# Kernel optimization log

Hardware: AMD Instinct MI355X
Metric: run time of the kernel (lower is better)

The kernel has to match this reference:

```python
import jax, jax.numpy as jnp
import numpy as np

_D4_CODESZ = 4
_N_VECS = 1048576  # 2^20 4-dim vectors (~ one large LLM weight matrix shard)


def _code3_signs(i3, x):
    x = list(x)
    if i3 & (1 << 5):
        x[2] *= -1
    if i3 & (1 << 6):
        x[1] *= -1
    if sum(x) % 2 != 0:
        x[3] *= -1
    if i3 & (1 << 7):
        x = [-v for v in x]
    assert sum(x) % 2 == 0
    return x


def _code8_to_d4(i8):
    assert 0 <= i8 < 256
    i3 = i8 & (7 << 5)
    i8 = i8 & 31
    if i8 < 16:
        if i8 < 8:
            if i8 < 2:
                if i8 < 1:
                    return _code3_signs(i3, [0.5] * _D4_CODESZ)
                else:
                    return _code3_signs(i3, [1.5] * _D4_CODESZ)
            else:
                ibx = i8 >> 1
                if i8 & 1:
                    x = [0.5] * _D4_CODESZ
                    x[0] = 1.5
                    x[ibx] = 1.5
                else:
                    x = [1.5] * _D4_CODESZ
                    x[0] = 0.5
                    x[ibx] = 0.5
                return _code3_signs(i3, x)
        else:
            ibx = i8 & 3
            if i8 < 8 + 4:
                x = [0.5] * _D4_CODESZ
                x[ibx] = 1.5
            else:
                x = [1.5] * _D4_CODESZ
                x[ibx] = 0.5
            return _code3_signs(i3, x)
    elif i8 < 16 + 4:
        ibx = i8 & 3
        x = [0.5] * _D4_CODESZ
        x[ibx] = 2.5
        return _code3_signs(i3, x)
    else:
        ibx = i8 - 20
        ib4 = ibx & 3
        ib3 = ibx >> 2
        x = [0.5] * _D4_CODESZ
        x[ib4] = 1.5
        if ib3 >= ib4:
            ib3 += 1
        x[ib3] = 2.5
        return _code3_signs(i3, x)


def _build_d4_grid():
    cb = np.zeros((256, _D4_CODESZ), dtype=np.float32)
    for i in range(256):
        cb[i] = _code8_to_d4(i)
    return cb


def setup_inputs() -> dict:
    key = jax.random.key(0)
    X = jax.random.normal(key, (_N_VECS, _D4_CODESZ), dtype=jnp.float32)
    grid = jnp.asarray(_build_d4_grid())            # [256, 4] D4 lattice codebook
    grid_norm = jnp.sum(grid * grid, axis=1)        # [256] squared norms
    return {"X": X, "grid": grid, "grid_norm": grid_norm}


def reference(X, grid, grid_norm):
    # nearest-codeword by argmax of 2<x,g> - |g|^2 (equiv. to min ||x-g||^2)
    scores = 2.0 * jnp.einsum("nd,kd->nk", X, grid) - grid_norm  # [N, 256]
    Xqidx = jnp.argmax(scores, axis=1)                           # [N]
    return grid[Xqidx], Xqidx.astype(jnp.uint8)
```

## Files before the change

### kernel.cpp

```cpp
#include <hip/hip_runtime.h>
#include <math.h>

#define THREADS 256

#define MCP_LIST \
  0x00, 0x55, 0x50, 0x05, 0x44, 0x11, 0x14, 0x41, \
  0x01, 0x04, 0x10, 0x40, 0x54, 0x51, 0x45, 0x15, \
  0x02, 0x08, 0x20, 0x80, 0x09, 0x06, 0x12, 0x42, \
  0x21, 0x24, 0x18, 0x48, 0x81, 0x84, 0x90, 0x60

__device__ const unsigned d_MCP[32] = { MCP_LIST };
constexpr unsigned h_MCP[32] = { MCP_LIST };

__global__ __launch_bounds__(THREADS)
void d4_fast_kernel(const float* __restrict__ X, float* __restrict__ out,
                    unsigned char* __restrict__ flags, int n)
{
    const int i = blockIdx.x * blockDim.x + threadIdx.x;
    if (i >= n) return;

    const float4 xv = reinterpret_cast<const float4*>(X)[i];
    const float fx0 = xv.x, fx1 = xv.y, fx2 = xv.z, fx3 = xv.w;

    const double a0 = fabs((double)fx0), a1 = fabs((double)fx1);
    const double a2 = fabs((double)fx2), a3 = fabs((double)fx3);
    const double u0 = a0 + a0, u1 = a1 + a1, u2 = a2 + a2, u3 = a3 + a3;
    const double v0 = u0 + u0, v1 = u1 + u1, v2 = u2 + u2, v3 = u3 + u3;
    const double h0 = 0.5 * a0, h1 = 0.5 * a1, h2 = 0.5 * a2, h3 = 0.5 * a3;
    const double t0 = h0 + a0, t1 = h1 + a1, t2 = h2 + a2, t3 = h3 + a3;
    const double w0 = t0 + a0, w1 = t1 + a1, w2 = t2 + a2, w3 = t3 + a3;
    const double A = (a0 + a1) + (a2 + a3);

    const int s0 = (fx0 < 0.f) ? 1 : 0, s1 = (fx1 < 0.f) ? 1 : 0;
    const int s2 = (fx2 < 0.f) ? 1 : 0, s3 = (fx3 < 0.f) ? 1 : 0;
    const int qp = (s0 + s1 + s2 + s3) & 1;

    double best = -1e300, second = -1e300;
    int bi = 0;
#pragma unroll
    for (int p = 0; p < 32; ++p) {
        const unsigned mc = h_MCP[p];
        const int c0 = mc & 3, c1 = (mc >> 2) & 3, c2 = (mc >> 4) & 3, c3 = (mc >> 6) & 3;
        const int nsq = 1 + c0 * (c0 + 1) + c1 * (c1 + 1) + c2 * (c2 + 1) + c3 * (c3 + 1);

        double s = A - (double)nsq;
        if (c0 == 1) s += u0; else if (c0 == 2) s += v0;
        if (c1 == 1) s += u1; else if (c1 == 2) s += v1;
        if (c2 == 1) s += u2; else if (c2 == 2) s += v2;
        if (c3 == 1) s += u3; else if (c3 == 2) s += v3;

        const double q0 = (c0 == 0) ? h0 : ((c0 == 1) ? t0 : w0);
        const double q1 = (c1 == 0) ? h1 : ((c1 == 1) ? t1 : w1);
        const double q2 = (c2 == 0) ? h2 : ((c2 == 1) ? t2 : w2);
        const double q3 = (c3 == 0) ? h3 : ((c3 == 1) ? t3 : w3);
        const double minp = fmin(fmin(q0, q1), fmin(q2, q3));

        const int rp = (c0 + c1 + c2 + c3) & 1;
        const double eff = (rp != qp) ? (s - 4.0 * minp) : s;

        if (eff > best) { second = best; best = eff; bi = p; }
        else if (eff > second) { second = eff; }
    }

    const unsigned mc = d_MCP[bi];
    const int c0 = mc & 3, c1 = (mc >> 2) & 3, c2 = (mc >> 4) & 3, c3 = (mc >> 6) & 3;
    const int rp = (c0 + c1 + c2 + c3) & 1;
    const bool flip = (rp != qp);

    const double p0 = (c0 == 0) ? h0 : ((c0 == 1) ? t0 : w0);
    const double p1 = (c1 == 0) ? h1 : ((c1 == 1) ? t1 : w1);
    const double p2 = (c2 == 0) ? h2 : ((c2 == 1) ? t2 : w2);
    const double p3 = (c3 == 0) ? h3 : ((c3 == 1) ? t3 : w3);
    int f = 0; double mp = p0;
    if (p1 < mp) { mp = p1; f = 1; }
    if (p2 < mp) { mp = p2; f = 2; }
    if (p3 < mp) { mp = p3; f = 3; }

    const double m01 = fmin(p0, p1), M01 = fmax(p0, p1);
    const double m23 = fmin(p2, p3), M23 = fmax(p2, p3);
    const double q1v = fmin(m01, m23);
    const double q2v = fmin(fmax(m01, m23), fmin(M01, M23));

    const double within = flip ? 4.0 * (q2v - q1v) : 4.0 * (q1v + q2v);
    const double gap = fmin(best - second, within);
    const double delta = 4e-6 * (A + 1.0);
    flags[i] = (gap < delta) ? 1 : 0;

    const bool n0 = ((s0 != 0) != (flip && f == 0));
    const bool n1 = ((s1 != 0) != (flip && f == 1));
    const bool n2 = ((s2 != 0) != (flip && f == 2));
    const bool n3 = ((s3 != 0) != (flip && f == 3));

    const float m0 = 0.5f + (float)c0, m1 = 0.5f + (float)c1;
    const float m2 = 0.5f + (float)c2, m3 = 0.5f + (float)c3;
    float4 g;
    g.x = n0 ? -m0 : m0;
    g.y = n1 ? -m1 : m1;
    g.z = n2 ? -m2 : m2;
    g.w = n3 ? -m3 : m3;

    const int b7 = n0 ? 1 : 0;
    const int b6 = (n1 ? 1 : 0) ^ b7;
    const int b5 = (n2 ? 1 : 0) ^ b7;
    const int idx = bi | (b5 << 5) | (b6 << 6) | (b7 << 7);

    reinterpret_cast<float4*>(out)[i] = g;
    out[(size_t)4 * (size_t)n + (size_t)i] = (float)idx;
}

__global__ __launch_bounds__(THREADS)
void d4_exact_kernel(const float* __restrict__ X,
                     const float* __restrict__ grid,
                     const float* __restrict__ gnorm,
                     float* __restrict__ out,
                     const unsigned char* __restrict__ flags, int n)
{
    const int i = blockIdx.x * blockDim.x + threadIdx.x;
    if (i >= n) return;
    if (!flags[i]) return;

    const float4 xv = reinterpret_cast<const float4*>(X)[i];
    float best = -INFINITY;
    int bk = 0;
    for (int k = 0; k < 256; ++k) {
        const float g0 = grid[4 * k + 0], g1 = grid[4 * k + 1];
        const float g2 = grid[4 * k + 2], g3 = grid[4 * k + 3];
        float d = __fmul_rn(xv.x, g0);
        d = __fadd_rn(d, __fmul_rn(xv.y, g1));
        d = __fadd_rn(d, __fmul_rn(xv.z, g2));
        d = __fadd_rn(d, __fmul_rn(xv.w, g3));
        const float s = __fsub_rn(__fmul_rn(2.0f, d), gnorm[k]);
        if (s > best) { best = s; bk = k; }
    }
    float4 g;
    g.x = grid[4 * bk + 0]; g.y = grid[4 * bk + 1];
    g.z = grid[4 * bk + 2]; g.w = grid[4 * bk + 3];
    reinterpret_cast<float4*>(out)[i] = g;
    out[(size_t)4 * (size_t)n + (size_t)i] = (float)bk;
}

extern "C" void kernel_launch(void* const* d_in, const int* in_sizes, int n_in,
                              void* d_out, int out_size, void* d_ws, size_t ws_size,
                              hipStream_t stream)
{
    const float* X = (const float*)d_in[0];
    const float* grid = (const float*)d_in[1];
    const float* gnorm = (const float*)d_in[2];
    float* out = (float*)d_out;
    unsigned char* flags = (unsigned char*)d_ws;
    const int n = in_sizes[0] / 4;
    const int blocks = (n + THREADS - 1) / THREADS;
    hipLaunchKernelGGL(d4_fast_kernel, dim3(blocks), dim3(THREADS), 0, stream,
                       X, out, flags, n);
    hipLaunchKernelGGL(d4_exact_kernel, dim3(blocks), dim3(THREADS), 0, stream,
                       X, grid, gnorm, out, flags, n);
}
```

Before: 107.6 us.

## Fuse fast and exact D4 quantizer kernels, switch to fp32, cache grid in LDS

Merges the fast lattice-decode kernel and the exact fallback kernel into one launch, so the flag buffer write/read and the second pass over X disappear. The heuristic scoring moves from double to float with a widened tie tolerance, and the codebook plus norms are staged in shared memory for the brute-force fallback. The risks are warp divergence when a few lanes take the 256-iteration fallback, and a float-precision margin that may flag more or fewer near-ties.

New measurement: 89.75 us, median of 2. 1.2x faster.

```diff
diff --git a/kernel.cpp b/kernel.cpp
--- a/kernel.cpp
+++ b/kernel.cpp
@@ -13,130 +13,126 @@
 constexpr unsigned h_MCP[32] = { MCP_LIST };
 
 __global__ __launch_bounds__(THREADS)
-void d4_fast_kernel(const float* __restrict__ X, float* __restrict__ out,
-                    unsigned char* __restrict__ flags, int n)
+void d4_fused_kernel(const float* __restrict__ X,
+                     const float* __restrict__ grid,
+                     const float* __restrict__ gnorm,
+                     float* __restrict__ out, int n)
 {
+    __shared__ float4 sgrid[256];
+    __shared__ float  sgn[256];
+    sgrid[threadIdx.x] = reinterpret_cast<const float4*>(grid)[threadIdx.x];
+    sgn[threadIdx.x]   = gnorm[threadIdx.x];
+    __syncthreads();
+
     const int i = blockIdx.x * blockDim.x + threadIdx.x;
     if (i >= n) return;
 
     const float4 xv = reinterpret_cast<const float4*>(X)[i];
     const float fx0 = xv.x, fx1 = xv.y, fx2 = xv.z, fx3 = xv.w;
 
-    const double a0 = fabs((double)fx0), a1 = fabs((double)fx1);
-    const double a2 = fabs((double)fx2), a3 = fabs((double)fx3);
-    const double u0 = a0 + a0, u1 = a1 + a1, u2 = a2 + a2, u3 = a3 + a3;
-    const double v0 = u0 + u0, v1 = u1 + u1, v2 = u2 + u2, v3 = u3 + u3;
-    const double h0 = 0.5 * a0, h1 = 0.5 * a1, h2 = 0.5 * a2, h3 = 0.5 * a3;
-    const double t0 = h0 + a0, t1 = h1 + a1, t2 = h2 + a2, t3 = h3 + a3;
-    const double w0 = t0 + a0, w1 = t1 + a1, w2 = t2 + a2, w3 = t3 + a3;
-    const double A = (a0 + a1) + (a2 + a3);
+    const float a0 = fabsf(fx0), a1 = fabsf(fx1), a2 = fabsf(fx2), a3 = fabsf(fx3);
+    const float r0 = (a0 + a0) - 2.f, r1 = (a1 + a1) - 2.f;
+    const float r2 = (a2 + a2) - 2.f, r3 = (a3 + a3) - 2.f;
+    const float z0 = (a0 + a0 + a0 + a0) - 6.f, z1 = (a1 + a1 + a1 + a1) - 6.f;
+    const float z2 = (a2 + a2 + a2 + a2) - 6.f, z3 = (a3 + a3 + a3 + a3) - 6.f;
+    const float A = (a0 + a1) + (a2 + a3);
+    const float base = A - 1.f;
+
+    const float h0 = 0.5f * a0, h1 = 0.5f * a1, h2 = 0.5f * a2, h3 = 0.5f * a3;
+    const float t0 = h0 + a0, t1 = h1 + a1, t2 = h2 + a2, t3 = h3 + a3;
+    const float w0 = t0 + a0, w1 = t1 + a1, w2 = t2 + a2, w3 = t3 + a3;
 
     const int s0 = (fx0 < 0.f) ? 1 : 0, s1 = (fx1 < 0.f) ? 1 : 0;
     const int s2 = (fx2 < 0.f) ? 1 : 0, s3 = (fx3 < 0.f) ? 1 : 0;
     const int qp = (s0 + s1 + s2 + s3) & 1;
 
-    double best = -1e300, second = -1e300;
+    float best = -1e30f, second = -1e30f;
     int bi = 0;
 #pragma unroll
     for (int p = 0; p < 32; ++p) {
         const unsigned mc = h_MCP[p];
         const int c0 = mc & 3, c1 = (mc >> 2) & 3, c2 = (mc >> 4) & 3, c3 = (mc >> 6) & 3;
-        const int nsq = 1 + c0 * (c0 + 1) + c1 * (c1 + 1) + c2 * (c2 + 1) + c3 * (c3 + 1);
 
-        double s = A - (double)nsq;
-        if (c0 == 1) s += u0; else if (c0 == 2) s += v0;
-        if (c1 == 1) s += u1; else if (c1 == 2) s += v1;
-        if (c2 == 1) s += u2; else if (c2 == 2) s += v2;
-        if (c3 == 1) s += u3; else if (c3 == 2) s += v3;
+        float s = base;
+        if (c0 == 1) s += r0; else if (c0 == 2) s += z0;
+        if (c1 == 1) s += r1; else if (c1 == 2) s += z1;
+        if (c2 == 1) s += r2; else if (c2 == 2) s += z2;
+        if (c3 == 1) s += r3; else if (c3 == 2) s += z3;
 
-        const double q0 = (c0 == 0) ? h0 : ((c0 == 1) ? t0 : w0);
-        const double q1 = (c1 == 0) ? h1 : ((c1 == 1) ? t1 : w1);
-        const double q2 = (c2 == 0) ? h2 : ((c2 == 1) ? t2 : w2);
-        const double q3 = (c3 == 0) ? h3 : ((c3 == 1) ? t3 : w3);
-        const double minp = fmin(fmin(q0, q1), fmin(q2, q3));
+        const float q0 = (c0 == 0) ? h0 : ((c0 == 1) ? t0 : w0);
+        const float q1 = (c1 == 0) ? h1 : ((c1 == 1) ? t1 : w1);
+        const float q2 = (c2 == 0) ? h2 : ((c2 == 1) ? t2 : w2);
+        const float q3 = (c3 == 0) ? h3 : ((c3 == 1) ? t3 : w3);
+        const float minp = fminf(fminf(q0, q1), fminf(q2, q3));
 
         const int rp = (c0 + c1 + c2 + c3) & 1;
-        const double eff = (rp != qp) ? (s - 4.0 * minp) : s;
+        const float eff = (rp != qp) ? (s - 4.f * minp) : s;
 
         if (eff > best) { second = best; best = eff; bi = p; }
         else if (eff > second) { second = eff; }
     }
 
-    const unsigned mc = d_MCP[bi];
-    const int c0 = mc & 3, c1 = (mc >> 2) & 3, c2 = (mc >> 4) & 3, c3 = (mc >> 6) & 3;
-    const int rp = (c0 + c1 + c2 + c3) & 1;
-    const bool flip = (rp != qp);
+    {
+        const unsigned mc = d_MCP[bi];
+        const int c0 = mc & 3, c1 = (mc >> 2) & 3, c2 = (mc >> 4) & 3, c3 = (mc >> 6) & 3;
+        const int rp = (c0 + c1 + c2 + c3) & 1;
+        const bool flip = (rp != qp);
 
-    const double p0 = (c0 == 0) ? h0 : ((c0 == 1) ? t0 : w0);
-    const double p1 = (c1 == 0) ? h1 : ((c1 == 1) ? t1 : w1);
-    const double p2 = (c2 == 0) ? h2 : ((c2 == 1) ? t2 : w2);
-    const double p3 = (c3 == 0) ? h3 : ((c3 == 1) ? t3 : w3);
-    int f = 0; double mp = p0;
-    if (p1 < mp) { mp = p1; f = 1; }
-    if (p2 < mp) { mp = p2; f = 2; }
-    if (p3 < mp) { mp = p3; f = 3; }
+        const float p0 = (c0 == 0) ? h0 : ((c0 == 1) ? t0 : w0);
+        const float p1 = (c1 == 0) ? h1 : ((c1 == 1) ? t1 : w1);
+        const float p2 = (c2 == 0) ? h2 : ((c2 == 1) ? t2 : w2);
+        const float p3 = (c3 == 0) ? h3 : ((c3 == 1) ? t3 : w3);
+        int f = 0; float mp = p0;
+        if (p1 < mp) { mp = p1; f = 1; }
+        if (p2 < mp) { mp = p2; f = 2; }
+        if (p3 < mp) { mp = p3; f = 3; }
 
-    const double m01 = fmin(p0, p1), M01 = fmax(p0, p1);
-    const double m23 = fmin(p2, p3), M23 = fmax(p2, p3);
-    const double q1v = fmin(m01, m23);
-    const double q2v = fmin(fmax(m01, m23), fmin(M01, M23));
+        const float m01 = fminf(p0, p1), M01 = fmaxf(p0, p1);
+        const float m23 = fminf(p2, p3), M23 = fmaxf(p2, p3);
+        const float q1v = fminf(m01, m23);
+        const float q2v = fminf(fmaxf(m01, m23), fminf(M01, M23));
 
-    const double within = flip ? 4.0 * (q2v - q1v) : 4.0 * (q1v + q2v);
-    const double gap = fmin(best - second, within);
-    const double delta = 4e-6 * (A + 1.0);
-    flags[i] = (gap < delta) ? 1 : 0;
+        const float within = flip ? 4.f * (q2v - q1v) : 4.f * (q1v + q2v);
+        const float gap = fminf(best - second, within);
+        const float delta = 8e-6f * (A + 6.f);
 
-    const bool n0 = ((s0 != 0) != (flip && f == 0));
-    const bool n1 = ((s1 != 0) != (flip && f == 1));
-    const bool n2 = ((s2 != 0) != (flip && f == 2));
-    const bool n3 = ((s3 != 0) != (flip && f == 3));
+        const bool n0 = ((s0 != 0) != (flip && f == 0));
+        const bool n1 = ((s1 != 0) != (flip && f == 1));
+        const bool n2 = ((s2 != 0) != (flip && f == 2));
+        const bool n3 = ((s3 != 0) != (flip && f == 3));
 
-    const float m0 = 0.5f + (float)c0, m1 = 0.5f + (float)c1;
-    const float m2 = 0.5f + (float)c2, m3 = 0.5f + (float)c3;
-    float4 g;
-    g.x = n0 ? -m0 : m0;
-    g.y = n1 ? -m1 : m1;
-    g.z = n2 ? -m2 : m2;
-    g.w = n3 ? -m3 : m3;
+        const float m0 = 0.5f + (float)c0, m1 = 0.5f + (float)c1;
+        const float m2 = 0.5f + (float)c2, m3 = 0.5f + (float)c3;
+        float4 g;
+        g.x = n0 ? -m0 : m0;
+        g.y = n1 ? -m1 : m1;
+        g.z = n2 ? -m2 : m2;
+        g.w = n3 ? -m3 : m3;
 
-    const int b7 = n0 ? 1 : 0;
-    const int b6 = (n1 ? 1 : 0) ^ b7;
-    const int b5 = (n2 ? 1 : 0) ^ b7;
-    const int idx = bi | (b5 << 5) | (b6 << 6) | (b7 << 7);
+        const int b7 = n0 ? 1 : 0;
+        const int b6 = (n1 ? 1 : 0) ^ b7;
+        const int b5 = (n2 ? 1 : 0) ^ b7;
+        int idx = bi | (b5 << 5) | (b6 << 6) | (b7 << 7);
 
-    reinterpret_cast<float4*>(out)[i] = g;
-    out[(size_t)4 * (size_t)n + (size_t)i] = (float)idx;
-}
+        if (gap < delta) {
+            float bexact = -INFINITY;
+            int bk = 0;
+            for (int k = 0; k < 256; ++k) {
+                const float4 gk = sgrid[k];
+                float d = __fmul_rn(fx0, gk.x);
+                d = __fadd_rn(d, __fmul_rn(fx1, gk.y));
+                d = __fadd_rn(d, __fmul_rn(fx2, gk.z));
+                d = __fadd_rn(d, __fmul_rn(fx3, gk.w));
+                const float sc = __fsub_rn(__fmul_rn(2.0f, d), sgn[k]);
+                if (sc > bexact) { bexact = sc; bk = k; }
+            }
+            g = sgrid[bk];
+            idx = bk;
+        }
 
-__global__ __launch_bounds__(THREADS)
-void d4_exact_kernel(const float* __restrict__ X,
-                     const float* __restrict__ grid,
-                     const float* __restrict__ gnorm,
-                     float* __restrict__ out,
-                     const unsigned char* __restrict__ flags, int n)
-{
-    const int i = blockIdx.x * blockDim.x + threadIdx.x;
-    if (i >= n) return;
-    if (!flags[i]) return;
-
-    const float4 xv = reinterpret_cast<const float4*>(X)[i];
-    float best = -INFINITY;
-    int bk = 0;
-    for (int k = 0; k < 256; ++k) {
-        const float g0 = grid[4 * k + 0], g1 = grid[4 * k + 1];
-        const float g2 = grid[4 * k + 2], g3 = grid[4 * k + 3];
-        float d = __fmul_rn(xv.x, g0);
-        d = __fadd_rn(d, __fmul_rn(xv.y, g1));
-        d = __fadd_rn(d, __fmul_rn(xv.z, g2));
-        d = __fadd_rn(d, __fmul_rn(xv.w, g3));
-        const float s = __fsub_rn(__fmul_rn(2.0f, d), gnorm[k]);
-        if (s > best) { best = s; bk = k; }
+        reinterpret_cast<float4*>(out)[i] = g;
+        out[(size_t)4 * (size_t)n + (size_t)i] = (float)idx;
     }
-    float4 g;
-    g.x = grid[4 * bk + 0]; g.y = grid[4 * bk + 1];
-    g.z = grid[4 * bk + 2]; g.w = grid[4 * bk + 3];
-    reinterpret_cast<float4*>(out)[i] = g;
-    out[(size_t)4 * (size_t)n + (size_t)i] = (float)bk;
 }
 
 extern "C" void kernel_launch(void* const* d_in, const int* in_sizes, int n_in,
@@ -147,11 +143,8 @@
     const float* grid = (const float*)d_in[1];
     const float* gnorm = (const float*)d_in[2];
     float* out = (float*)d_out;
-    unsigned char* flags = (unsigned char*)d_ws;
     const int n = in_sizes[0] / 4;
     const int blocks = (n + THREADS - 1) / THREADS;
-    hipLaunchKernelGGL(d4_fast_kernel, dim3(blocks), dim3(THREADS), 0, stream,
-                       X, out, flags, n);
-    hipLaunchKernelGGL(d4_exact_kernel, dim3(blocks), dim3(THREADS), 0, stream,
-                       X, grid, gnorm, out, flags, n);
+    hipLaunchKernelGGL(d4_fused_kernel, dim3(blocks), dim3(THREADS), 0, stream,
+                       X, grid, gnorm, out, n);
 }
```
